# Kernel optimization log

Hardware: AMD Instinct MI355X
Metric: run time of the kernel (lower is better)

Reference implementation:

```python
import jax, jax.numpy as jnp
import numpy as np
import math

H = 8          # num_heads
DV = 1024      # dim_V
LN_EPS = 1e-5


def _layernorm(x, g, b):
    mu = jnp.mean(x, axis=-1, keepdims=True)
    var = jnp.mean(jnp.square(x - mu), axis=-1, keepdims=True)
    return (x - mu) * jax.lax.rsqrt(var + LN_EPS) * g + b


def setup_inputs() -> dict:
    key = jax.random.key(0)
    ks = jax.random.split(key, 12)
    B, NQ, NK, DQ, DK = 4, 2048, 2048, 1024, 1024
    s = 0.02
    return {
        "Q": jax.random.normal(ks[0], (B, NQ, DQ), jnp.float32),
        "K": jax.random.normal(ks[1], (B, NK, DK), jnp.float32),
        "Wq": jax.random.normal(ks[2], (DV, DQ), jnp.float32) * s,
        "bq": jnp.zeros((DV,), jnp.float32),
        "Wk": jax.random.normal(ks[3], (DV, DK), jnp.float32) * s,
        "bk": jnp.zeros((DV,), jnp.float32),
        "Wv": jax.random.normal(ks[4], (DV, DK), jnp.float32) * s,
        "bv": jnp.zeros((DV,), jnp.float32),
        "Wo": jax.random.normal(ks[5], (DV, DV), jnp.float32) * s,
        "bo": jnp.zeros((DV,), jnp.float32),
        "g0": jnp.ones((DV,), jnp.float32),
        "b0": jnp.zeros((DV,), jnp.float32),
        "g1": jnp.ones((DV,), jnp.float32),
        "b1": jnp.zeros((DV,), jnp.float32),
    }


def reference(Q, K, Wq, bq, Wk, bk, Wv, bv, Wo, bo, g0, b0, g1, b1):
    B, NQ, _ = Q.shape
    NK = K.shape[1]
    d = DV // H  # per-head dim
    # projections
    q = (Q @ Wq.T + bq).reshape(B, NQ, H, d)
    k = (K @ Wk.T + bk).reshape(B, NK, H, d)
    v = (K @ Wv.T + bv).reshape(B, NK, H, d)
    # attention per head (split along feature dim == head split in torch code)
    logits = jnp.einsum('bqhd,bkhd->bhqk', q, k) / math.sqrt(d)
    A = jax.nn.softmax(logits, axis=-1)
    o = q + jnp.einsum('bhqk,bkhd->bqhd', A, v)  # residual with projected Q
    O = o.reshape(B, NQ, DV)
    O = _layernorm(O, g0, b0)
    O = O + jax.nn.relu(O @ Wo.T + bo)
    O = _layernorm(O, g1, b1)
    return O
```

## Files before the change

### kernel.cpp

```cpp
#include <hip/hip_runtime.h>
#include <hip/hip_bf16.h>

typedef __bf16 bf16_t;
typedef __bf16 bf16x8 __attribute__((ext_vector_type(8)));
typedef __bf16 bf16x4 __attribute__((ext_vector_type(4)));
typedef float f32x4 __attribute__((ext_vector_type(4)));

#define B_DIM 4
#define NQ 2048
#define NK 2048
#define DMODEL 1024
#define NH 8
#define DHEAD 128

#define AS1 __attribute__((address_space(1)))
#define AS3 __attribute__((address_space(3)))

__device__ __forceinline__ void gl_lds16(const void* g, void* l) {
    __builtin_amdgcn_global_load_lds((const AS1 void*)g, (AS3 void*)l, 16, 0, 0);
}

struct CvtArgs {
    const float* s[6];
    bf16_t* d[6];
    int n[6];
};

__global__ __launch_bounds__(256) void cvt_k(CvtArgs a) {
    const int p = blockIdx.y;
    const float* s = a.s[p];
    bf16_t* d = a.d[p];
    const int n = a.n[p];
    const int stride = gridDim.x * 256 * 8;
    for (int i = (blockIdx.x * 256 + threadIdx.x) * 8; i < n; i += stride) {
        float4 x0 = *(const float4*)(s + i);
        float4 x1 = *(const float4*)(s + i + 4);
        bf16x8 o = {(bf16_t)x0.x, (bf16_t)x0.y, (bf16_t)x0.z, (bf16_t)x0.w,
                    (bf16_t)x1.x, (bf16_t)x1.y, (bf16_t)x1.z, (bf16_t)x1.w};
        *(bf16x8*)(d + i) = o;
    }
}

__global__ __launch_bounds__(256) void proj_k(
    const bf16_t* Qc, const bf16_t* Kc,
    const bf16_t* Wqc, const bf16_t* Wkc, const bf16_t* Wvc,
    const float* bq, const float* bk, const float* bv,
    bf16_t* qbb, bf16_t* kbb, bf16_t* vT)
{
    const int K = DMODEL, N = DMODEL;
    const int z = blockIdx.z;
    const bf16_t* A  = (z == 0) ? Qc : Kc;
    const bf16_t* Bw = (z == 0) ? Wqc : (z == 1) ? Wkc : Wvc;
    const float* bias = (z == 0) ? bq : (z == 1) ? bk : bv;
    bf16_t* Cb = (z == 0) ? qbb : (z == 1) ? kbb : vT;

    const int tid  = threadIdx.x;
    const int lane = tid & 63;
    const int wv   = tid >> 6;
    const int l16  = lane & 15;
    const int quad = (lane >> 4) & 3;
    const int kc4  = lane >> 4;
    const int wr   = wv >> 1, wc = wv & 1;
    const int rowBase = blockIdx.y * 128;
    const int colBase = blockIdx.x * 128;

    __shared__ bf16_t sA[4096];
    __shared__ bf16_t sB[4096];

    const bf16_t* gA = A + (size_t)(rowBase + wv * 32 + l16) * K + kc4 * 8;
    const bf16_t* gB = Bw + (size_t)(colBase + wv * 32 + l16) * K + kc4 * 8;
    bf16_t* lA0 = &sA[(wv * 2) * 512];
    bf16_t* lA1 = &sA[(wv * 2 + 1) * 512];
    bf16_t* lB0 = &sB[(wv * 2) * 512];
    bf16_t* lB1 = &sB[(wv * 2 + 1) * 512];

    const f32x4 fz = {0.f, 0.f, 0.f, 0.f};
    f32x4 acc[4][4];
#pragma unroll
    for (int i = 0; i < 4; i++)
#pragma unroll
        for (int j = 0; j < 4; j++) acc[i][j] = fz;

    for (int k0 = 0; k0 < K; k0 += 32) {
        gl_lds16(gA, lA0);
        gl_lds16(gA + (size_t)16 * K, lA1);
        gl_lds16(gB, lB0);
        gl_lds16(gB + (size_t)16 * K, lB1);
        gA += 32; gB += 32;
        __syncthreads();

        bf16x8 aF[4], bF[4];
#pragma unroll
        for (int mi = 0; mi < 4; mi++)
            aF[mi] = *(const bf16x8*)(&sA[(wr * 4 + mi) * 512 + (quad * 16 + l16) * 8]);
#pragma unroll
        for (int ni = 0; ni < 4; ni++)
            bF[ni] = *(const bf16x8*)(&sB[(wc * 4 + ni) * 512 + (quad * 16 + l16) * 8]);
#pragma unroll
        for (int mi = 0; mi < 4; mi++)
#pragma unroll
            for (int ni = 0; ni < 4; ni++)
                acc[mi][ni] = __builtin_amdgcn_mfma_f32_16x16x32_bf16(
                    aF[mi], bF[ni], acc[mi][ni], 0, 0, 0);
        __syncthreads();
    }

#pragma unroll
    for (int mi = 0; mi < 4; mi++) {
#pragma unroll
        for (int ni = 0; ni < 4; ni++) {
            int row0 = rowBase + wr * 64 + mi * 16 + quad * 4;
            int col  = colBase + wc * 64 + ni * 16 + l16;
            float bvv = bias[col];
            if (z != 2) {
#pragma unroll
                for (int r = 0; r < 4; r++)
                    Cb[(size_t)(row0 + r) * N + col] = (bf16_t)(acc[mi][ni][r] + bvv);
            } else {
                int b  = row0 >> 11;
                int n0 = row0 & 2047;
                int hh = col >> 7;
                int dd = col & 127;
                bf16x4 p = {(bf16_t)(acc[mi][ni][0] + bvv), (bf16_t)(acc[mi][ni][1] + bvv),
                            (bf16_t)(acc[mi][ni][2] + bvv), (bf16_t)(acc[mi][ni][3] + bvv)};
                *(bf16x4*)(Cb + (size_t)((b * NH + hh) * DHEAD + dd) * NK + n0) = p;
            }
        }
    }
}

__global__ __launch_bounds__(256) void gemm_wo(
    const bf16_t* __restrict__ A, const bf16_t* __restrict__ Bw,
    const float* __restrict__ bias, const float* resid, float* Cf, int M, int N, int K)
{
    const int tid  = threadIdx.x;
    const int lane = tid & 63;
    const int wv   = tid >> 6;
    const int l16  = lane & 15;
    const int quad = (lane >> 4) & 3;
    const int kc4  = lane >> 4;
    const int wr   = wv >> 1, wc = wv & 1;
    const int rowBase = blockIdx.y * 128;
    const int colBase = blockIdx.x * 128;

    __shared__ bf16_t sA[4096];
    __shared__ bf16_t sB[4096];

    const bf16_t* gA = A + (size_t)(rowBase + wv * 32 + l16) * K + kc4 * 8;
    const bf16_t* gB = Bw + (size_t)(colBase + wv * 32 + l16) * K + kc4 * 8;
    bf16_t* lA0 = &sA[(wv * 2) * 512];
    bf16_t* lA1 = &sA[(wv * 2 + 1) * 512];
    bf16_t* lB0 = &sB[(wv * 2) * 512];
    bf16_t* lB1 = &sB[(wv * 2 + 1) * 512];

    const f32x4 fz = {0.f, 0.f, 0.f, 0.f};
    f32x4 acc[4][4];
#pragma unroll
    for (int i = 0; i < 4; i++)
#pragma unroll
        for (int j = 0; j < 4; j++) acc[i][j] = fz;

    for (int k0 = 0; k0 < K; k0 += 32) {
        gl_lds16(gA, lA0);
        gl_lds16(gA + (size_t)16 * K, lA1);
        gl_lds16(gB, lB0);
        gl_lds16(gB + (size_t)16 * K, lB1);
        gA += 32; gB += 32;
        __syncthreads();

        bf16x8 aF[4], bF[4];
#pragma unroll
        for (int mi = 0; mi < 4; mi++)
            aF[mi] = *(const bf16x8*)(&sA[(wr * 4 + mi) * 512 + (quad * 16 + l16) * 8]);
#pragma unroll
        for (int ni = 0; ni < 4; ni++)
            bF[ni] = *(const bf16x8*)(&sB[(wc * 4 + ni) * 512 + (quad * 16 + l16) * 8]);
#pragma unroll
        for (int mi = 0; mi < 4; mi++)
#pragma unroll
            for (int ni = 0; ni < 4; ni++)
                acc[mi][ni] = __builtin_amdgcn_mfma_f32_16x16x32_bf16(
                    aF[mi], bF[ni], acc[mi][ni], 0, 0, 0);
        __syncthreads();
    }

#pragma unroll
    for (int mi = 0; mi < 4; mi++) {
#pragma unroll
        for (int ni = 0; ni < 4; ni++) {
            int row0 = rowBase + wr * 64 + mi * 16 + quad * 4;
            int col  = colBase + wc * 64 + ni * 16 + l16;
            float bvv = bias[col];
#pragma unroll
            for (int r = 0; r < 4; r++) {
                float v = acc[mi][ni][r] + bvv;
                v = v > 0.f ? v : 0.f;
                Cf[(size_t)(row0 + r) * N + col] =
                    resid[(size_t)(row0 + r) * N + col] + v;
            }
        }
    }
}

__global__ __launch_bounds__(128, 2) void attn_k(
    const bf16_t* __restrict__ qb, const bf16_t* __restrict__ kb,
    const bf16_t* __restrict__ vT, float* __restrict__ O)
{
    const int tid  = threadIdx.x;
    const int lane = tid & 63;
    const int wv   = tid >> 6;
    const int l16  = lane & 15;
    const int quad = (lane >> 4) & 3;
    const int bh   = blockIdx.x;
    const int b    = bh >> 3;
    const int h    = bh & 7;
    const int qt   = blockIdx.y * 64;
    const int qrow0 = b * NQ + qt + wv * 32;

    __shared__ bf16_t sK[8192];
    __shared__ bf16_t sV[8192];

    bf16x8 qF[2][4];
#pragma unroll
    for (int qq = 0; qq < 2; qq++)
#pragma unroll
        for (int c = 0; c < 4; c++)
            qF[qq][c] = *(const bf16x8*)(qb + (size_t)(qrow0 + qq * 16 + l16) * DMODEL +
                                         h * DHEAD + c * 32 + quad * 8);

    const f32x4 fz = {0.f, 0.f, 0.f, 0.f};
    f32x4 accO[8][2];
#pragma unroll
    for (int db = 0; db < 8; db++)
#pragma unroll
        for (int qq = 0; qq < 2; qq++) accO[db][qq] = fz;
    float mq[2] = {-3e38f, -3e38f};
    float lq[2] = {0.f, 0.f};
    const float SC2 = 0.08838834764831845f * 1.44269504089f;

    const bf16_t* gKb = kb + ((size_t)b * NK + l16) * DMODEL + h * DHEAD + quad * 8;
    const bf16_t* gVb = vT + ((size_t)bh * DHEAD + l16) * NK + quad * 8;
    const int qa   = (quad & 1) * 2;
    const int srcA = l16 + 16 * qa;
    const int srcB = srcA + 16;
    const bool hi  = (quad >> 1) != 0;

    for (int kt = 0; kt < NK; kt += 64) {
#pragma unroll
        for (int kb2 = 0; kb2 < 2; kb2++) {
            const int kbi = wv * 2 + kb2;
#pragma unroll
            for (int c = 0; c < 4; c++)
                gl_lds16(gKb + (size_t)(kt + kbi * 16) * DMODEL + c * 32,
                         &sK[(kbi * 4 + c) * 512]);
        }
#pragma unroll
        for (int db2 = 0; db2 < 4; db2++) {
            const int dbi = wv * 4 + db2;
#pragma unroll
            for (int kc = 0; kc < 2; kc++)
                gl_lds16(gVb + (size_t)(dbi * 16) * NK + kt + kc * 32,
                         &sV[(dbi * 2 + kc) * 512]);
        }
        __syncthreads();

        f32x4 S[4][2];
#pragma unroll
        for (int kb4 = 0; kb4 < 4; kb4++) {
            S[kb4][0] = fz; S[kb4][1] = fz;
#pragma unroll
            for (int c = 0; c < 4; c++) {
                bf16x8 kF = *(const bf16x8*)(&sK[(kb4 * 4 + c) * 512 + lane * 8]);
                S[kb4][0] = __builtin_amdgcn_mfma_f32_16x16x32_bf16(kF, qF[0][c], S[kb4][0], 0, 0, 0);
                S[kb4][1] = __builtin_amdgcn_mfma_f32_16x16x32_bf16(kF, qF[1][c], S[kb4][1], 0, 0, 0);
            }
        }

        float alph[2];
#pragma unroll
        for (int qq = 0; qq < 2; qq++) {
            float mx = fmaxf(fmaxf(fmaxf(S[0][qq][0], S[0][qq][1]), fmaxf(S[0][qq][2], S[0][qq][3])),
                       fmaxf(fmaxf(S[1][qq][0], S[1][qq][1]), fmaxf(S[1][qq][2], S[1][qq][3])));
            mx = fmaxf(mx, fmaxf(fmaxf(fmaxf(S[2][qq][0], S[2][qq][1]), fmaxf(S[2][qq][2], S[2][qq][3])),
                           fmaxf(fmaxf(S[3][qq][0], S[3][qq][1]), fmaxf(S[3][qq][2], S[3][qq][3]))));
            mx = fmaxf(mx, __shfl_xor(mx, 16));
            mx = fmaxf(mx, __shfl_xor(mx, 32));
            float mn = fmaxf(mq[qq], mx);
            float al = exp2f((mq[qq] - mn) * SC2);
            mq[qq] = mn;
            float mc = mn * SC2;
            float sum = 0.f;
#pragma unroll
            for (int kb4 = 0; kb4 < 4; kb4++)
#pragma unroll
                for (int r = 0; r < 4; r++) {
                    float p = exp2f(fmaf(S[kb4][qq][r], SC2, -mc));
                    S[kb4][qq][r] = p;
                    sum += p;
                }
            lq[qq] = lq[qq] * al + sum;
            alph[qq] = al;
        }
#pragma unroll
        for (int db = 0; db < 8; db++)
#pragma unroll
            for (int qq = 0; qq < 2; qq++)
#pragma unroll
                for (int r = 0; r < 4; r++) accO[db][qq][r] *= alph[qq];

        uint2 pk[4][2];
#pragma unroll
        for (int kb4 = 0; kb4 < 4; kb4++)
#pragma unroll
            for (int qq = 0; qq < 2; qq++) {
                bf16x4 t = {(bf16_t)S[kb4][qq][0], (bf16_t)S[kb4][qq][1],
                            (bf16_t)S[kb4][qq][2], (bf16_t)S[kb4][qq][3]};
                pk[kb4][qq] = __builtin_bit_cast(uint2, t);
            }
        bf16x8 pF[2][2];
#pragma unroll
        for (int kc = 0; kc < 2; kc++)
#pragma unroll
            for (int qq = 0; qq < 2; qq++) {
                unsigned a0 = (unsigned)__shfl((int)pk[2 * kc][qq].x, srcA);
                unsigned b0 = (unsigned)__shfl((int)pk[2 * kc + 1][qq].x, srcA);
                unsigned a1 = (unsigned)__shfl((int)pk[2 * kc][qq].y, srcA);
                unsigned b1 = (unsigned)__shfl((int)pk[2 * kc + 1][qq].y, srcA);
                unsigned a2 = (unsigned)__shfl((int)pk[2 * kc][qq].x, srcB);
                unsigned b2 = (unsigned)__shfl((int)pk[2 * kc + 1][qq].x, srcB);
                unsigned a3 = (unsigned)__shfl((int)pk[2 * kc][qq].y, srcB);
                unsigned b3 = (unsigned)__shfl((int)pk[2 * kc + 1][qq].y, srcB);
                uint4 w = {hi ? b0 : a0, hi ? b1 : a1, hi ? b2 : a2, hi ? b3 : a3};
                pF[kc][qq] = __builtin_bit_cast(bf16x8, w);
            }

#pragma unroll
        for (int kc = 0; kc < 2; kc++)
#pragma unroll
            for (int db = 0; db < 8; db++) {
                bf16x8 vF = *(const bf16x8*)(&sV[(db * 2 + kc) * 512 + lane * 8]);
                accO[db][0] = __builtin_amdgcn_mfma_f32_16x16x32_bf16(vF, pF[kc][0], accO[db][0], 0, 0, 0);
                accO[db][1] = __builtin_amdgcn_mfma_f32_16x16x32_bf16(vF, pF[kc][1], accO[db][1], 0, 0, 0);
            }
        __syncthreads();
    }

    float inv[2];
#pragma unroll
    for (int qq = 0; qq < 2; qq++) {
        float s = lq[qq];
        s += __shfl_xor(s, 16);
        s += __shfl_xor(s, 32);
        inv[qq] = 1.0f / s;
    }

#pragma unroll
    for (int qq = 0; qq < 2; qq++) {
        const int grow = qrow0 + qq * 16 + l16;
#pragma unroll
        for (int db = 0; db < 8; db++) {
            const int gcol = h * DHEAD + db * 16 + quad * 4;
            bf16x4 qr = *(const bf16x4*)(qb + (size_t)grow * DMODEL + gcol);
            f32x4 o;
#pragma unroll
            for (int r = 0; r < 4; r++)
                o[r] = accO[db][qq][r] * inv[qq] + (float)qr[r];
            *(f32x4*)(O + (size_t)grow * DMODEL + gcol) = o;
        }
    }
}

__global__ __launch_bounds__(256) void ln_k(
    const float* __restrict__ X, const float* __restrict__ g,
    const float* __restrict__ bta, float* __restrict__ Yf, bf16_t* Yb)
{
    const int row = blockIdx.x;
    const int t = threadIdx.x;
    float4 x = *(const float4*)(X + (size_t)row * DMODEL + t * 4);
    float s  = x.x + x.y + x.z + x.w;
    float sq = x.x * x.x + x.y * x.y + x.z * x.z + x.w * x.w;
#pragma unroll
    for (int o = 1; o < 64; o <<= 1) {
        s  += __shfl_xor(s, o);
        sq += __shfl_xor(sq, o);
    }
    __shared__ float ls[8];
    int w = t >> 6, ln = t & 63;
    if (ln == 0) { ls[w] = s; ls[4 + w] = sq; }
    __syncthreads();
    s  = ls[0] + ls[1] + ls[2] + ls[3];
    sq = ls[4] + ls[5] + ls[6] + ls[7];
    float mu  = s * (1.f / DMODEL);
    float var = sq * (1.f / DMODEL) - mu * mu;
    float rs  = rsqrtf(var + 1e-5f);
    float4 gv = *(const float4*)(g + t * 4);
    float4 bv = *(const float4*)(bta + t * 4);
    float4 y;
    y.x = (x.x - mu) * rs * gv.x + bv.x;
    y.y = (x.y - mu) * rs * gv.y + bv.y;
    y.z = (x.z - mu) * rs * gv.z + bv.z;
    y.w = (x.w - mu) * rs * gv.w + bv.w;
    *(float4*)(Yf + (size_t)row * DMODEL + t * 4) = y;
    if (Yb) {
        bf16x4 yb = {(bf16_t)y.x, (bf16_t)y.y, (bf16_t)y.z, (bf16_t)y.w};
        *(bf16x4*)(Yb + (size_t)row * DMODEL + t * 4) = yb;
    }
}

extern "C" void kernel_launch(void* const* d_in, const int* in_sizes, int n_in,
                              void* d_out, int out_size, void* d_ws, size_t ws_size,
                              hipStream_t stream)
{
    const float* Q  = (const float*)d_in[0];
    const float* Kx = (const float*)d_in[1];
    const float* Wq = (const float*)d_in[2];
    const float* bq = (const float*)d_in[3];
    const float* Wk = (const float*)d_in[4];
    const float* bk = (const float*)d_in[5];
    const float* Wv = (const float*)d_in[6];
    const float* bv = (const float*)d_in[7];
    const float* Wo = (const float*)d_in[8];
    const float* bo = (const float*)d_in[9];
    const float* g0 = (const float*)d_in[10];
    const float* b0 = (const float*)d_in[11];
    const float* g1 = (const float*)d_in[12];
    const float* b1 = (const float*)d_in[13];
    float* out = (float*)d_out;

    char* ws = (char*)d_ws;
    bf16_t* Qc  = (bf16_t*)(ws);
    bf16_t* Kc  = (bf16_t*)(ws + 16777216);
    bf16_t* Wqc = (bf16_t*)(ws + 33554432);
    bf16_t* Wkc = (bf16_t*)(ws + 35651584);
    bf16_t* Wvc = (bf16_t*)(ws + 37748736);
    bf16_t* Woc = (bf16_t*)(ws + 39845888);
    bf16_t* qbb = (bf16_t*)(ws + 41943040);
    bf16_t* kbb = (bf16_t*)(ws + 58720256);
    bf16_t* vT  = (bf16_t*)(ws + 75497472);
    float*  Obuf = (float*)(ws + 92274688);
    float*  Lf  = (float*)(ws);
    bf16_t* Lb  = kbb;

    CvtArgs ca;
    ca.s[0] = Q;  ca.d[0] = Qc;  ca.n[0] = B_DIM * NQ * DMODEL;
    ca.s[1] = Kx; ca.d[1] = Kc;  ca.n[1] = B_DIM * NK * DMODEL;
    ca.s[2] = Wq; ca.d[2] = Wqc; ca.n[2] = DMODEL * DMODEL;
    ca.s[3] = Wk; ca.d[3] = Wkc; ca.n[3] = DMODEL * DMODEL;
    ca.s[4] = Wv; ca.d[4] = Wvc; ca.n[4] = DMODEL * DMODEL;
    ca.s[5] = Wo; ca.d[5] = Woc; ca.n[5] = DMODEL * DMODEL;
    cvt_k<<<dim3(512, 6), 256, 0, stream>>>(ca);

    const int M = B_DIM * NQ;

    proj_k<<<dim3(DMODEL / 128, M / 128, 3), 256, 0, stream>>>(
        Qc, Kc, Wqc, Wkc, Wvc, bq, bk, bv, qbb, kbb, vT);

    attn_k<<<dim3(B_DIM * NH, NQ / 64), 128, 0, stream>>>(qbb, kbb, vT, Obuf);

    ln_k<<<dim3(M), 256, 0, stream>>>(Obuf, g0, b0, Lf, Lb);

    gemm_wo<<<dim3(DMODEL / 128, M / 128), 256, 0, stream>>>(
        Lb, Woc, bo, Lf, Lf, M, DMODEL, DMODEL);

    ln_k<<<dim3(M), 256, 0, stream>>>(Lf, g1, b1, out, nullptr);
}
```

Before: 459.7 us.

## Double-buffer K/V tiles in attention, use 4 waves per block, add setprio

The attention kernel now uses 256 threads covering 128 query rows per block, so each K/V tile load is shared across twice as many waves. K/V tiles are double-buffered in LDS, and the next tile is prefetched while the current one is computed, which removes one barrier per iteration and hides global-to-LDS latency. MFMA sections are wrapped in s_setprio to favour matrix issue. LDS use doubles to 64KB per block, which may reduce occupancy, and the grid has half as many blocks.

New measurement: 441.9 us. -3.9%, faster.

```diff
diff --git a/kernel.cpp b/kernel.cpp
--- a/kernel.cpp
+++ b/kernel.cpp
@@ -202,7 +202,7 @@
     }
 }
 
-__global__ __launch_bounds__(128, 2) void attn_k(
+__global__ __launch_bounds__(256, 2) void attn_k(
     const bf16_t* __restrict__ qb, const bf16_t* __restrict__ kb,
     const bf16_t* __restrict__ vT, float* __restrict__ O)
 {
@@ -214,11 +214,31 @@
     const int bh   = blockIdx.x;
     const int b    = bh >> 3;
     const int h    = bh & 7;
-    const int qt   = blockIdx.y * 64;
+    const int qt   = blockIdx.y * 128;
     const int qrow0 = b * NQ + qt + wv * 32;
 
-    __shared__ bf16_t sK[8192];
-    __shared__ bf16_t sV[8192];
+    __shared__ bf16_t sK[2][8192];
+    __shared__ bf16_t sV[2][8192];
+
+    const bf16_t* gKb = kb + ((size_t)b * NK + l16) * DMODEL + h * DHEAD + quad * 8;
+    const bf16_t* gVb = vT + ((size_t)bh * DHEAD + l16) * NK + quad * 8;
+
+    auto stage = [&](int kt, int bufi) {
+#pragma unroll
+        for (int c = 0; c < 4; c++)
+            gl_lds16(gKb + (size_t)(kt + wv * 16) * DMODEL + c * 32,
+                     &sK[bufi][(wv * 4 + c) * 512]);
+#pragma unroll
+        for (int d2 = 0; d2 < 2; d2++) {
+            const int dbi = wv * 2 + d2;
+#pragma unroll
+            for (int kc = 0; kc < 2; kc++)
+                gl_lds16(gVb + (size_t)(dbi * 16) * NK + kt + kc * 32,
+                         &sV[bufi][(dbi * 2 + kc) * 512]);
+        }
+    };
+
+    stage(0, 0);
 
     bf16x8 qF[2][4];
 #pragma unroll
@@ -238,43 +258,30 @@
     float lq[2] = {0.f, 0.f};
     const float SC2 = 0.08838834764831845f * 1.44269504089f;
 
-    const bf16_t* gKb = kb + ((size_t)b * NK + l16) * DMODEL + h * DHEAD + quad * 8;
-    const bf16_t* gVb = vT + ((size_t)bh * DHEAD + l16) * NK + quad * 8;
     const int qa   = (quad & 1) * 2;
     const int srcA = l16 + 16 * qa;
     const int srcB = srcA + 16;
     const bool hi  = (quad >> 1) != 0;
 
+    __syncthreads();
+    int cur = 0;
+
     for (int kt = 0; kt < NK; kt += 64) {
-#pragma unroll
-        for (int kb2 = 0; kb2 < 2; kb2++) {
-            const int kbi = wv * 2 + kb2;
-#pragma unroll
-            for (int c = 0; c < 4; c++)
-                gl_lds16(gKb + (size_t)(kt + kbi * 16) * DMODEL + c * 32,
-                         &sK[(kbi * 4 + c) * 512]);
-        }
-#pragma unroll
-        for (int db2 = 0; db2 < 4; db2++) {
-            const int dbi = wv * 4 + db2;
-#pragma unroll
-            for (int kc = 0; kc < 2; kc++)
-                gl_lds16(gVb + (size_t)(dbi * 16) * NK + kt + kc * 32,
-                         &sV[(dbi * 2 + kc) * 512]);
-        }
-        __syncthreads();
+        if (kt + 64 < NK) stage(kt + 64, cur ^ 1);
 
         f32x4 S[4][2];
+        __builtin_amdgcn_s_setprio(1);
 #pragma unroll
         for (int kb4 = 0; kb4 < 4; kb4++) {
             S[kb4][0] = fz; S[kb4][1] = fz;
 #pragma unroll
             for (int c = 0; c < 4; c++) {
-                bf16x8 kF = *(const bf16x8*)(&sK[(kb4 * 4 + c) * 512 + lane * 8]);
+                bf16x8 kF = *(const bf16x8*)(&sK[cur][(kb4 * 4 + c) * 512 + lane * 8]);
                 S[kb4][0] = __builtin_amdgcn_mfma_f32_16x16x32_bf16(kF, qF[0][c], S[kb4][0], 0, 0, 0);
                 S[kb4][1] = __builtin_amdgcn_mfma_f32_16x16x32_bf16(kF, qF[1][c], S[kb4][1], 0, 0, 0);
             }
         }
+        __builtin_amdgcn_s_setprio(0);
 
         float alph[2];
 #pragma unroll
@@ -334,15 +341,19 @@
                 pF[kc][qq] = __builtin_bit_cast(bf16x8, w);
             }
 
+        __builtin_amdgcn_s_setprio(1);
 #pragma unroll
         for (int kc = 0; kc < 2; kc++)
 #pragma unroll
             for (int db = 0; db < 8; db++) {
-                bf16x8 vF = *(const bf16x8*)(&sV[(db * 2 + kc) * 512 + lane * 8]);
+                bf16x8 vF = *(const bf16x8*)(&sV[cur][(db * 2 + kc) * 512 + lane * 8]);
                 accO[db][0] = __builtin_amdgcn_mfma_f32_16x16x32_bf16(vF, pF[kc][0], accO[db][0], 0, 0, 0);
                 accO[db][1] = __builtin_amdgcn_mfma_f32_16x16x32_bf16(vF, pF[kc][1], accO[db][1], 0, 0, 0);
             }
+        __builtin_amdgcn_s_setprio(0);
+
         __syncthreads();
+        cur ^= 1;
     }
 
     float inv[2];
@@ -455,7 +466,7 @@
     proj_k<<<dim3(DMODEL / 128, M / 128, 3), 256, 0, stream>>>(
         Qc, Kc, Wqc, Wkc, Wvc, bq, bk, bv, qbb, kbb, vT);
 
-    attn_k<<<dim3(B_DIM * NH, NQ / 64), 128, 0, stream>>>(qbb, kbb, vT, Obuf);
+    attn_k<<<dim3(B_DIM * NH, NQ / 128), 256, 0, stream>>>(qbb, kbb, vT, Obuf);
 
     ln_k<<<dim3(M), 256, 0, stream>>>(Obuf, g0, b0, Lf, Lb);
 
```
